# Kernel tuning notes

Measured on AMD Instinct MI355X. Metric: run time of the kernel, lower is better.

Reference implementation:

```python
import jax, jax.numpy as jnp
import numpy as np

N_NODES = 50000
N_EDGES = 400000
H = 64          # node hidden state dim (entities_dimensions['node'])
E_DIM = 8       # edge_params dim (message.extra_parameters)
MSG_HID = 128   # message-creation MLP hidden width
RD_HID = 128    # readout hidden width
T = 2           # message-passing steps


def setup_inputs() -> dict:
    key = jax.random.key(0)
    ks = jax.random.split(key, 12)
    def w(k, shape):
        return jax.random.normal(k, shape, dtype=jnp.float32) * 0.05
    return {
        "node_feats": jax.random.normal(ks[0], (N_NODES, H), dtype=jnp.float32),
        "edge_feats": jax.random.normal(ks[1], (N_EDGES, E_DIM), dtype=jnp.float32),
        "edge_src": jax.random.randint(ks[2], (N_EDGES,), 0, N_NODES),
        "edge_dst": jax.random.randint(ks[3], (N_EDGES,), 0, N_NODES),
        # message creation MLP: concat(hs_src, hs_dst, edge_params) -> relu -> H
        "W_msg1": w(ks[4], (2 * H + E_DIM, MSG_HID)),
        "b_msg1": jnp.zeros((MSG_HID,), jnp.float32),
        "W_msg2": w(ks[5], (MSG_HID, H)),
        "b_msg2": jnp.zeros((H,), jnp.float32),
        # GRU cell update (keras GRUCell convention, reset_after=False)
        "W_x": w(ks[6], (H, 3 * H)),
        "W_h": w(ks[7], (H, 3 * H)),
        "b_gru": jnp.zeros((3 * H,), jnp.float32),
        # readout MLP: H -> relu -> 1
        "W_r1": w(ks[8], (H, RD_HID)),
        "b_r1": jnp.zeros((RD_HID,), jnp.float32),
        "W_r2": w(ks[9], (RD_HID, 1)),
        "b_r2": jnp.zeros((1,), jnp.float32),
    }


def _gru_cell(h, x, W_x, W_h, b):
    # gates order: update (z), reset (r), candidate (h~) — keras convention
    gx = x @ W_x + b
    gh = h @ W_h
    xz, xr, xh = jnp.split(gx, 3, axis=-1)
    hz, hr, hh = jnp.split(gh, 3, axis=-1)
    z = jax.nn.sigmoid(xz + hz)
    r = jax.nn.sigmoid(xr + hr)
    hc = jnp.tanh(xh + r * hh)
    return z * h + (1.0 - z) * hc


def reference(node_feats, edge_feats, edge_src, edge_dst,
              W_msg1, b_msg1, W_msg2, b_msg2,
              W_x, W_h, b_gru, W_r1, b_r1, W_r2, b_r2):
    h = node_feats  # [N, H] hidden states initialized from entity features
    for _ in range(T):
        # gather source/destination node states per edge: [E, H]
        src_h = h[edge_src]
        dst_h = h[edge_dst]
        m_in = jnp.concatenate([src_h, dst_h, edge_feats], axis=-1)  # [E, 2H+E_DIM]
        m = jax.nn.relu(m_in @ W_msg1 + b_msg1) @ W_msg2 + b_msg2    # [E, H]
        # scatter-sum aggregation to destination nodes: [N, H]
        agg = jax.ops.segment_sum(m, edge_dst, num_segments=N_NODES)
        # recurrent (GRU) node-state update
        h = _gru_cell(h, agg, W_x, W_h, b_gru)
    # readout MLP on final hidden states
    out = jax.nn.relu(h @ W_r1 + b_r1) @ W_r2 + b_r2  # [N, 1]
    return out
```

## Files before the change

kernel.cpp:

```cpp
#include <hip/hip_runtime.h>
#include <hip/hip_bf16.h>

#define NN 50000
#define NE 400000
#define NPAIR 12500
#define NCH 196
#define NPAD 50176

typedef __bf16 bf16_t;
typedef __bf16 bf16x4 __attribute__((ext_vector_type(4)));
typedef __bf16 bf16x8 __attribute__((ext_vector_type(8)));
typedef float  floatx4 __attribute__((ext_vector_type(4)));

static __device__ __forceinline__ floatx4 mfma16(bf16x8 a, bf16x8 b, floatx4 c) {
    return __builtin_amdgcn_mfma_f32_16x16x32_bf16(a, b, c, 0, 0, 0);
}
static __device__ __forceinline__ float sigm_f(float x) {
    return 1.f / (1.f + __expf(-x));
}
static __device__ __forceinline__ float tanh_f(float x) {
    return 1.f - 2.f / (__expf(2.f * x) + 1.f);
}
static __device__ __forceinline__ bf16x8 cvt8(const float* sp) {
    float4 f0 = *(const float4*)sp;
    float4 f1 = *(const float4*)(sp + 4);
    bf16x8 v;
    v[0] = (bf16_t)f0.x; v[1] = (bf16_t)f0.y; v[2] = (bf16_t)f0.z; v[3] = (bf16_t)f0.w;
    v[4] = (bf16_t)f1.x; v[5] = (bf16_t)f1.y; v[6] = (bf16_t)f1.z; v[7] = (bf16_t)f1.w;
    return v;
}

__global__ __launch_bounds__(256) void prep_kernel(
    const float* __restrict__ nf,
    const float* __restrict__ Wm1, const float* __restrict__ Wm2,
    const float* __restrict__ Wx,  const float* __restrict__ Wh,
    const float* __restrict__ Wr1,
    bf16_t* __restrict__ hb,
    bf16_t* __restrict__ W1f, bf16_t* __restrict__ W2f,
    bf16_t* __restrict__ Wxt, bf16_t* __restrict__ Wht,
    bf16_t* __restrict__ Wr1f)
{
    int u = blockIdx.x * 256 + threadIdx.x;
    if (u < 800000) {
        float4 v = *(const float4*)(nf + (size_t)u * 4);
        bf16x4 o;
        o[0] = (bf16_t)v.x; o[1] = (bf16_t)v.y; o[2] = (bf16_t)v.z; o[3] = (bf16_t)v.w;
        *(bf16x4*)(hb + (size_t)u * 4) = o;
        return;
    }
    u -= 800000;
    if (u < 20480) {
        int j = u & 7, l = (u >> 3) & 63, rem = u >> 9;
        int ks = rem % 5, nt = rem / 5;
        int n = nt * 16 + (l & 15);
        int k = ks * 32 + (l >> 4) * 8 + j;
        W1f[u] = (k < 136) ? (bf16_t)Wm1[k * 128 + n] : (bf16_t)0.f;
        return;
    }
    u -= 20480;
    if (u < 8192) {
        int j = u & 7, l = (u >> 3) & 63, rem = u >> 9;
        int kg = rem & 3, nt = rem >> 2;
        int n = nt * 16 + (l & 15);
        int k = kg * 32 + (l >> 4) * 8 + j;
        W2f[u] = (bf16_t)Wm2[k * 64 + n];
        return;
    }
    u -= 8192;
    if (u < 12288) {
        int n = u >> 6, k = u & 63;
        Wxt[u] = (bf16_t)Wx[k * 192 + n];
        return;
    }
    u -= 12288;
    if (u < 12288) {
        int n = u >> 6, k = u & 63;
        Wht[u] = (bf16_t)Wh[k * 192 + n];
        return;
    }
    u -= 12288;
    if (u < 8192) {
        int j = u & 7, l = (u >> 3) & 63, rem = u >> 9;
        int kg = rem & 1, nt = rem >> 1;
        int n = nt * 16 + (l & 15);
        int k = kg * 32 + (l >> 4) * 8 + j;
        Wr1f[u] = (bf16_t)Wr1[k * 128 + n];
    }
}

__global__ __launch_bounds__(256) void hist_kernel(
    const int* __restrict__ edst, int* __restrict__ deg)
{
    int e = blockIdx.x * 256 + threadIdx.x;
    if (e < NE) atomicAdd(&deg[edst[e]], 1);
}

__global__ __launch_bounds__(256) void scanA_kernel(
    const int* __restrict__ deg, int* __restrict__ chunkSums)
{
    __shared__ int s[256];
    int i = blockIdx.x * 256 + threadIdx.x;
    s[threadIdx.x] = deg[i];
    __syncthreads();
    for (int st = 128; st >= 1; st >>= 1) {
        if (threadIdx.x < st) s[threadIdx.x] += s[threadIdx.x + st];
        __syncthreads();
    }
    if (threadIdx.x == 0) chunkSums[blockIdx.x] = s[0];
}

__global__ __launch_bounds__(256) void scanB_kernel(
    const int* __restrict__ chunkSums, int* __restrict__ chunkOff)
{
    __shared__ int s[256];
    int t = threadIdx.x;
    int v = (t < NCH) ? chunkSums[t] : 0;
    s[t] = v;
    __syncthreads();
    for (int st = 1; st < 256; st <<= 1) {
        int add = (t >= st) ? s[t - st] : 0;
        __syncthreads();
        s[t] += add;
        __syncthreads();
    }
    if (t < NCH) chunkOff[t] = s[t] - v;
}

__global__ __launch_bounds__(256) void scanC_kernel(
    const int* __restrict__ deg, const int* __restrict__ chunkOff,
    int* __restrict__ cursor)
{
    __shared__ int s[256];
    int t = threadIdx.x;
    int i = blockIdx.x * 256 + t;
    int v = deg[i];
    s[t] = v;
    __syncthreads();
    for (int st = 1; st < 256; st <<= 1) {
        int add = (t >= st) ? s[t - st] : 0;
        __syncthreads();
        s[t] += add;
        __syncthreads();
    }
    cursor[i] = chunkOff[blockIdx.x] + s[t] - v;
}

__global__ __launch_bounds__(256) void scatter_kernel(
    const int* __restrict__ esrc, const int* __restrict__ edst,
    const float* __restrict__ ef,
    int* __restrict__ cursor, int* __restrict__ srcs, int* __restrict__ dsts,
    bf16_t* __restrict__ efpb)
{
    int e = blockIdx.x * 256 + threadIdx.x;
    if (e >= NE) return;
    int d = edst[e];
    int p = atomicAdd(&cursor[d], 1);
    srcs[p] = esrc[e];
    dsts[p] = d;
    float4 a = *(const float4*)(ef + (size_t)e * 8);
    float4 b = *(const float4*)(ef + (size_t)e * 8 + 4);
    bf16x8 v;
    v[0] = (bf16_t)a.x; v[1] = (bf16_t)a.y; v[2] = (bf16_t)a.z; v[3] = (bf16_t)a.w;
    v[4] = (bf16_t)b.x; v[5] = (bf16_t)b.y; v[6] = (bf16_t)b.z; v[7] = (bf16_t)b.w;
    *(bf16x8*)(efpb + (size_t)p * 8) = v;
}

__global__ __launch_bounds__(256) void edge_kernel(
    const bf16_t* __restrict__ hb, const bf16_t* __restrict__ efpb,
    const int* __restrict__ srcs, const int* __restrict__ dsts,
    const bf16_t* __restrict__ W1f, const bf16_t* __restrict__ W2f,
    const float* __restrict__ b1f, const float* __restrict__ b2f,
    bf16_t* __restrict__ mb)
{
    __shared__ __attribute__((aligned(16))) bf16_t w1s[20480];
    __shared__ __attribute__((aligned(16))) bf16_t w2s[8192];
    __shared__ __attribute__((aligned(16))) bf16_t hq[4][32 * 36];

    const int tid = threadIdx.x;
    {
        const uint4* s1 = (const uint4*)W1f;
        uint4* d1 = (uint4*)w1s;
        #pragma unroll
        for (int i = 0; i < 10; i++) d1[tid + i * 256] = s1[tid + i * 256];
        const uint4* s2 = (const uint4*)W2f;
        uint4* d2 = (uint4*)w2s;
        #pragma unroll
        for (int i = 0; i < 4; i++) d2[tid + i * 256] = s2[tid + i * 256];
    }
    __syncthreads();

    const int lane = tid & 63;
    const int wv   = tid >> 6;
    const int l15  = lane & 15;
    const int quad = lane >> 4;

    float b1r[8], b2r[4];
    #pragma unroll
    for (int nt = 0; nt < 8; nt++) b1r[nt] = b1f[nt * 16 + l15];
    #pragma unroll
    for (int nt = 0; nt < 4; nt++) b2r[nt] = b2f[nt * 16 + l15];

    const int WTOT = gridDim.x * 4;

    auto LDIDX = [&](int pp, int* idx) {
        int b = pp * 32;
        idx[0] = srcs[b + l15];       idx[1] = dsts[b + l15];
        idx[2] = srcs[b + 16 + l15];  idx[3] = dsts[b + 16 + l15];
    };
    auto GATHER = [&](const int* idx, int pp, bf16x8* af) {
        const bf16_t* sp0 = hb + (size_t)idx[0] * 64 + quad * 8;
        const bf16_t* dp0 = hb + (size_t)idx[1] * 64 + quad * 8;
        const bf16_t* sp1 = hb + (size_t)idx[2] * 64 + quad * 8;
        const bf16_t* dp1 = hb + (size_t)idx[3] * 64 + quad * 8;
        af[0] = *(const bf16x8*)sp0;  af[1] = *(const bf16x8*)(sp0 + 32);
        af[2] = *(const bf16x8*)dp0;  af[3] = *(const bf16x8*)(dp0 + 32);
        af[5] = *(const bf16x8*)sp1;  af[6] = *(const bf16x8*)(sp1 + 32);
        af[7] = *(const bf16x8*)dp1;  af[8] = *(const bf16x8*)(dp1 + 32);
        if (quad == 0) {
            int b = pp * 32;
            af[4] = *(const bf16x8*)(efpb + (size_t)(b + l15) * 8);
            af[9] = *(const bf16x8*)(efpb + (size_t)(b + 16 + l15) * 8);
        }
    };
    auto COMPSTORE = [&](const bf16x8* af, int pcur) {
        floatx4 oa0[4], oa1[4];
        #pragma unroll
        for (int nt = 0; nt < 4; nt++) {
            oa0[nt].x=0.f; oa0[nt].y=0.f; oa0[nt].z=0.f; oa0[nt].w=0.f;
            oa1[nt].x=0.f; oa1[nt].y=0.f; oa1[nt].z=0.f; oa1[nt].w=0.f;
        }
        #pragma unroll
        for (int q = 0; q < 4; q++) {
            floatx4 ac0[2], ac1[2];
            #pragma unroll
            for (int nt = 0; nt < 2; nt++) {
                ac0[nt].x=0.f; ac0[nt].y=0.f; ac0[nt].z=0.f; ac0[nt].w=0.f;
                ac1[nt].x=0.f; ac1[nt].y=0.f; ac1[nt].z=0.f; ac1[nt].w=0.f;
            }
            #pragma unroll
            for (int nt = 0; nt < 2; nt++) {
                int gnt = q * 2 + nt;
                #pragma unroll
                for (int ks = 0; ks < 5; ks++) {
                    bf16x8 b = *(const bf16x8*)(w1s + ((gnt * 5 + ks) * 64 + lane) * 8);
                    ac0[nt] = mfma16(af[ks], b, ac0[nt]);
                    ac1[nt] = mfma16(af[5 + ks], b, ac1[nt]);
                }
            }
            #pragma unroll
            for (int nt = 0; nt < 2; nt++) {
                float bb = b1r[q * 2 + nt];
                #pragma unroll
                for (int r = 0; r < 4; r++) {
                    float v0 = fmaxf(ac0[nt][r] + bb, 0.f);
                    float v1 = fmaxf(ac1[nt][r] + bb, 0.f);
                    hq[wv][(quad * 4 + r) * 36 + nt * 16 + l15]      = (bf16_t)v0;
                    hq[wv][(16 + quad * 4 + r) * 36 + nt * 16 + l15] = (bf16_t)v1;
                }
            }
            bf16x8 hf0 = *(const bf16x8*)(hq[wv] + l15 * 36 + quad * 8);
            bf16x8 hf1 = *(const bf16x8*)(hq[wv] + (16 + l15) * 36 + quad * 8);
            #pragma unroll
            for (int nt = 0; nt < 4; nt++) {
                bf16x8 w2 = *(const bf16x8*)(w2s + ((nt * 4 + q) * 64 + lane) * 8);
                oa0[nt] = mfma16(hf0, w2, oa0[nt]);
                oa1[nt] = mfma16(hf1, w2, oa1[nt]);
            }
        }
        int base = pcur * 32;
        #pragma unroll
        for (int nt = 0; nt < 4; nt++) {
            int col = nt * 16 + l15;
            float bb = b2r[nt];
            #pragma unroll
            for (int r = 0; r < 4; r++) {
                int row0 = base + quad * 4 + r;
                int row1 = base + 16 + quad * 4 + r;
                mb[(size_t)row0 * 64 + col] = (bf16_t)(oa0[nt][r] + bb);
                mb[(size_t)row1 * 64 + col] = (bf16_t)(oa1[nt][r] + bb);
            }
        }
    };

    int p = blockIdx.x * 4 + wv;
    int iA[4], iB[4];
    bf16x8 afA[10], afB[10];
    if (quad != 0) {
        #pragma unroll
        for (int q = 0; q < 8; q++) {
            afA[4][q] = (bf16_t)0.f; afA[9][q] = (bf16_t)0.f;
            afB[4][q] = (bf16_t)0.f; afB[9][q] = (bf16_t)0.f;
        }
    }

    LDIDX(p, iA);
    GATHER(iA, p, afA);
    int pn = p + WTOT;
    int pp = (pn < NPAIR) ? pn : p;
    LDIDX(pp, iB);

    while (true) {
        GATHER(iB, pp, afB);
        {
            int pn2 = pn + WTOT;
            int pq  = (pn2 < NPAIR) ? pn2 : pp;
            LDIDX(pq, iA);
            COMPSTORE(afA, p);
            if (pn >= NPAIR) break;
            p = pn; pn = pn2; pp = pq;
        }
        GATHER(iA, pp, afA);
        {
            int pn2 = pn + WTOT;
            int pq  = (pn2 < NPAIR) ? pn2 : pp;
            LDIDX(pq, iB);
            COMPSTORE(afB, p);
            if (pn >= NPAIR) break;
            p = pn; pn = pn2; pp = pq;
        }
    }
}

__global__ __launch_bounds__(256) void agg_kernel(
    const bf16_t* __restrict__ mb, const int* __restrict__ deg,
    const int* __restrict__ cursor, bf16_t* __restrict__ aggb)
{
    const int node = blockIdx.x * 4 + (threadIdx.x >> 6);
    if (node >= NN) return;
    const int lane = threadIdx.x & 63;
    int dg  = deg[node];
    int end = cursor[node];
    int st  = end - dg;
    float s0 = 0.f, s1 = 0.f;
    int e = st;
    for (; e + 1 < end; e += 2) {
        s0 += (float)mb[(size_t)e * 64 + lane];
        s1 += (float)mb[(size_t)(e + 1) * 64 + lane];
    }
    if (e < end) s0 += (float)mb[(size_t)e * 64 + lane];
    aggb[(size_t)node * 64 + lane] = (bf16_t)(s0 + s1);
}

template<int LAST>
__global__ __launch_bounds__(256) void gru_kernel(
    const bf16_t* __restrict__ aggb, const float* __restrict__ h_in,
    float* __restrict__ h_out, bf16_t* __restrict__ hb_out,
    const bf16_t* __restrict__ Wxt, const bf16_t* __restrict__ Wht,
    const float* __restrict__ bg,
    const bf16_t* __restrict__ Wr1f, const float* __restrict__ br1,
    const float* __restrict__ Wr2, const float* __restrict__ br2,
    float* __restrict__ out)
{
    __shared__ __attribute__((aligned(16))) float  shd[64 * 68];
    __shared__ __attribute__((aligned(16))) bf16_t hb2[4][16 * 72];
    const int tid = threadIdx.x;
    const int n0  = blockIdx.x * 64;

    for (int idx = tid; idx < 64 * 16; idx += 256) {
        int i = idx >> 4, c = (idx & 15) * 4;
        int n = n0 + i; if (n >= NN) n = NN - 1;
        *(float4*)&shd[i * 68 + c] = *(const float4*)(h_in + (size_t)n * 64 + c);
    }
    __syncthreads();

    const int lane = tid & 63;
    const int wv   = tid >> 6;
    const int l15  = lane & 15;
    const int quad = lane >> 4;
    const int rowA = wv * 16 + l15;
    int nA = n0 + rowA; if (nA >= NN) nA = NN - 1;

    bf16x8 ax[2], ah[2];
    ax[0] = *(const bf16x8*)(aggb + (size_t)nA * 64 + quad * 8);
    ax[1] = *(const bf16x8*)(aggb + (size_t)nA * 64 + quad * 8 + 32);
    {
        const float* hp = shd + rowA * 68 + quad * 8;
        ah[0] = cvt8(hp);
        ah[1] = cvt8(hp + 32);
    }

    floatx4 az[4], ar[4], axh[4], ahh[4];
    #pragma unroll
    for (int nt = 0; nt < 4; nt++) {
        az[nt].x=0.f; az[nt].y=0.f; az[nt].z=0.f; az[nt].w=0.f;
        ar[nt].x=0.f; ar[nt].y=0.f; ar[nt].z=0.f; ar[nt].w=0.f;
        axh[nt].x=0.f; axh[nt].y=0.f; axh[nt].z=0.f; axh[nt].w=0.f;
        ahh[nt].x=0.f; ahh[nt].y=0.f; ahh[nt].z=0.f; ahh[nt].w=0.f;
    }
    #pragma unroll
    for (int nt = 0; nt < 4; nt++) {
        const bf16_t* bx_z = Wxt + (nt * 16 + l15) * 64 + quad * 8;
        const bf16_t* bh_z = Wht + (nt * 16 + l15) * 64 + quad * 8;
        const bf16_t* bx_r = bx_z + 64 * 64;
        const bf16_t* bh_r = bh_z + 64 * 64;
        const bf16_t* bx_h = bx_z + 128 * 64;
        const bf16_t* bh_h = bh_z + 128 * 64;
        az[nt]  = mfma16(ax[0], *(const bf16x8*)bx_z,        az[nt]);
        az[nt]  = mfma16(ax[1], *(const bf16x8*)(bx_z + 32), az[nt]);
        az[nt]  = mfma16(ah[0], *(const bf16x8*)bh_z,        az[nt]);
        az[nt]  = mfma16(ah[1], *(const bf16x8*)(bh_z + 32), az[nt]);
        ar[nt]  = mfma16(ax[0], *(const bf16x8*)bx_r,        ar[nt]);
        ar[nt]  = mfma16(ax[1], *(const bf16x8*)(bx_r + 32), ar[nt]);
        ar[nt]  = mfma16(ah[0], *(const bf16x8*)bh_r,        ar[nt]);
        ar[nt]  = mfma16(ah[1], *(const bf16x8*)(bh_r + 32), ar[nt]);
        axh[nt] = mfma16(ax[0], *(const bf16x8*)bx_h,        axh[nt]);
        axh[nt] = mfma16(ax[1], *(const bf16x8*)(bx_h + 32), axh[nt]);
        ahh[nt] = mfma16(ah[0], *(const bf16x8*)bh_h,        ahh[nt]);
        ahh[nt] = mfma16(ah[1], *(const bf16x8*)(bh_h + 32), ahh[nt]);
    }

    #pragma unroll
    for (int nt = 0; nt < 4; nt++) {
        int j = nt * 16 + l15;
        float bz = bg[j], brr = bg[64 + j], bh = bg[128 + j];
        #pragma unroll
        for (int r = 0; r < 4; r++) {
            int lrow = wv * 16 + quad * 4 + r;
            int n = n0 + lrow;
            float z  = sigm_f(az[nt][r] + bz);
            float rr = sigm_f(ar[nt][r] + brr);
            float hc = tanh_f(axh[nt][r] + bh + rr * ahh[nt][r]);
            float hold = shd[lrow * 68 + j];
            float hnew = z * hold + (1.f - z) * hc;
            if (LAST) {
                hb2[wv][(quad * 4 + r) * 72 + j] = (bf16_t)hnew;
            } else if (n < NN) {
                h_out[(size_t)n * 64 + j]  = hnew;
                hb_out[(size_t)n * 64 + j] = (bf16_t)hnew;
            }
        }
    }

    if (LAST) {
        bf16x8 a0 = *(const bf16x8*)(hb2[wv] + l15 * 72 + quad * 8);
        bf16x8 a1 = *(const bf16x8*)(hb2[wv] + l15 * 72 + quad * 8 + 32);
        floatx4 accR[8];
        #pragma unroll
        for (int nt = 0; nt < 8; nt++) { accR[nt].x=0.f; accR[nt].y=0.f; accR[nt].z=0.f; accR[nt].w=0.f; }
        #pragma unroll
        for (int nt = 0; nt < 8; nt++) {
            bf16x8 b0 = *(const bf16x8*)(Wr1f + ((nt * 2 + 0) * 64 + lane) * 8);
            bf16x8 b1 = *(const bf16x8*)(Wr1f + ((nt * 2 + 1) * 64 + lane) * 8);
            accR[nt] = mfma16(a0, b0, accR[nt]);
            accR[nt] = mfma16(a1, b1, accR[nt]);
        }
        float br1r[8], wr2r[8];
        #pragma unroll
        for (int nt = 0; nt < 8; nt++) {
            br1r[nt] = br1[nt * 16 + l15];
            wr2r[nt] = Wr2[nt * 16 + l15];
        }
        float br2v = br2[0];
        #pragma unroll
        for (int r = 0; r < 4; r++) {
            float p = 0.f;
            #pragma unroll
            for (int nt = 0; nt < 8; nt++)
                p += fmaxf(accR[nt][r] + br1r[nt], 0.f) * wr2r[nt];
            p += __shfl_xor(p, 1, 64);
            p += __shfl_xor(p, 2, 64);
            p += __shfl_xor(p, 4, 64);
            p += __shfl_xor(p, 8, 64);
            if (l15 == 0) {
                int n = n0 + wv * 16 + quad * 4 + r;
                if (n < NN) out[n] = p + br2v;
            }
        }
    }
}

extern "C" void kernel_launch(void* const* d_in, const int* in_sizes, int n_in,
                              void* d_out, int out_size, void* d_ws, size_t ws_size,
                              hipStream_t stream)
{
    const float* nf  = (const float*)d_in[0];
    const float* ef  = (const float*)d_in[1];
    const int* esrc  = (const int*)d_in[2];
    const int* edst  = (const int*)d_in[3];
    const float* Wm1 = (const float*)d_in[4];
    const float* bm1 = (const float*)d_in[5];
    const float* Wm2 = (const float*)d_in[6];
    const float* bm2 = (const float*)d_in[7];
    const float* Wx  = (const float*)d_in[8];
    const float* Wh  = (const float*)d_in[9];
    const float* bg  = (const float*)d_in[10];
    const float* Wr1 = (const float*)d_in[11];
    const float* br1 = (const float*)d_in[12];
    const float* Wr2 = (const float*)d_in[13];
    const float* br2 = (const float*)d_in[14];

    char* ws = (char*)d_ws;
    float*  hbuf   = (float*)(ws);
    bf16_t* hb     = (bf16_t*)(ws + 12800000);
    bf16_t* W1f    = (bf16_t*)(ws + 19200000);
    bf16_t* W2f    = (bf16_t*)(ws + 19240960);
    bf16_t* Wxt    = (bf16_t*)(ws + 19257344);
    bf16_t* Wht    = (bf16_t*)(ws + 19281920);
    bf16_t* Wr1f   = (bf16_t*)(ws + 19306496);
    int*    srcs   = (int*)(ws + 19322880);
    int*    dsts   = (int*)(ws + 20922880);
    bf16_t* efpb   = (bf16_t*)(ws + 22522880);
    int*    deg    = (int*)(ws + 28922880);
    int*    cursor = (int*)(ws + 29123584);
    int*    chunkS = (int*)(ws + 29324288);
    int*    chunkO = (int*)(ws + 29325312);
    bf16_t* aggb   = (bf16_t*)(ws + 29326336);
    bf16_t* mb     = (bf16_t*)(ws + 35726336);

    prep_kernel<<<3365, 256, 0, stream>>>(nf, Wm1, Wm2, Wx, Wh, Wr1,
                                          hb, W1f, W2f, Wxt, Wht, Wr1f);

    hipMemsetAsync(deg, 0, (size_t)NPAD * 4, stream);
    hist_kernel<<<(NE + 255) / 256, 256, 0, stream>>>(edst, deg);
    scanA_kernel<<<NCH, 256, 0, stream>>>(deg, chunkS);
    scanB_kernel<<<1, 256, 0, stream>>>(chunkS, chunkO);
    scanC_kernel<<<NCH, 256, 0, stream>>>(deg, chunkO, cursor);
    scatter_kernel<<<(NE + 255) / 256, 256, 0, stream>>>(esrc, edst, ef, cursor,
                                                         srcs, dsts, efpb);

    edge_kernel<<<1024, 256, 0, stream>>>(hb, efpb, srcs, dsts,
                                          W1f, W2f, bm1, bm2, mb);
    agg_kernel<<<(NN + 3) / 4, 256, 0, stream>>>(mb, deg, cursor, aggb);
    gru_kernel<0><<<(NN + 63) / 64, 256, 0, stream>>>(
        aggb, nf, hbuf, hb, Wxt, Wht, bg, Wr1f, br1, Wr2, br2, (float*)d_out);
    edge_kernel<<<1024, 256, 0, stream>>>(hb, efpb, srcs, dsts,
                                          W1f, W2f, bm1, bm2, mb);
    agg_kernel<<<(NN + 3) / 4, 256, 0, stream>>>(mb, deg, cursor, aggb);
    gru_kernel<1><<<(NN + 63) / 64, 256, 0, stream>>>(
        aggb, hbuf, nullptr, nullptr, Wxt, Wht, bg, Wr1f, br1, Wr2, br2,
        (float*)d_out);
}
```

Baseline: 318.5 us.

## Store messages in permuted column layout for vectorized writes and aggregation reads

The message-creation epilogue now stores each lane's four column-tile outputs as one contiguous bf16x4 write, which permutes the column order in the intermediate message buffer. The aggregation kernel reads that layout with 8-byte vector loads, gives each wave quarter a different edge, and combines the four partial sums with cross-lane shuffles before un-permuting on store. The goal is fewer, wider stores and loads on the message buffer plus more edges in flight per node. In exchange it adds a shuffle reduction, and three quarters of the lanes sit idle during the final store.

```diff
diff --git a/kernel.cpp b/kernel.cpp
--- a/kernel.cpp
+++ b/kernel.cpp
@@ -269,16 +269,20 @@
         }
         int base = pcur * 32;
         #pragma unroll
-        for (int nt = 0; nt < 4; nt++) {
-            int col = nt * 16 + l15;
-            float bb = b2r[nt];
-            #pragma unroll
-            for (int r = 0; r < 4; r++) {
-                int row0 = base + quad * 4 + r;
-                int row1 = base + 16 + quad * 4 + r;
-                mb[(size_t)row0 * 64 + col] = (bf16_t)(oa0[nt][r] + bb);
-                mb[(size_t)row1 * 64 + col] = (bf16_t)(oa1[nt][r] + bb);
-            }
+        for (int r = 0; r < 4; r++) {
+            int row0 = base + quad * 4 + r;
+            int row1 = base + 16 + quad * 4 + r;
+            bf16x4 t0, t1;
+            t0[0] = (bf16_t)(oa0[0][r] + b2r[0]);
+            t0[1] = (bf16_t)(oa0[1][r] + b2r[1]);
+            t0[2] = (bf16_t)(oa0[2][r] + b2r[2]);
+            t0[3] = (bf16_t)(oa0[3][r] + b2r[3]);
+            t1[0] = (bf16_t)(oa1[0][r] + b2r[0]);
+            t1[1] = (bf16_t)(oa1[1][r] + b2r[1]);
+            t1[2] = (bf16_t)(oa1[2][r] + b2r[2]);
+            t1[3] = (bf16_t)(oa1[3][r] + b2r[3]);
+            *(bf16x4*)(mb + (size_t)row0 * 64 + l15 * 4) = t0;
+            *(bf16x4*)(mb + (size_t)row1 * 64 + l15 * 4) = t1;
         }
     };
 
@@ -328,17 +332,26 @@
     const int node = blockIdx.x * 4 + (threadIdx.x >> 6);
     if (node >= NN) return;
     const int lane = threadIdx.x & 63;
+    const int l15  = lane & 15;
+    const int quad = lane >> 4;
     int dg  = deg[node];
     int end = cursor[node];
     int st  = end - dg;
-    float s0 = 0.f, s1 = 0.f;
-    int e = st;
-    for (; e + 1 < end; e += 2) {
-        s0 += (float)mb[(size_t)e * 64 + lane];
-        s1 += (float)mb[(size_t)(e + 1) * 64 + lane];
-    }
-    if (e < end) s0 += (float)mb[(size_t)e * 64 + lane];
-    aggb[(size_t)node * 64 + lane] = (bf16_t)(s0 + s1);
+    float a0 = 0.f, a1 = 0.f, a2 = 0.f, a3 = 0.f;
+    for (int e = st + quad; e < end; e += 4) {
+        bf16x4 v = *(const bf16x4*)(mb + (size_t)e * 64 + l15 * 4);
+        a0 += (float)v[0]; a1 += (float)v[1]; a2 += (float)v[2]; a3 += (float)v[3];
+    }
+    a0 += __shfl_xor(a0, 16, 64); a0 += __shfl_xor(a0, 32, 64);
+    a1 += __shfl_xor(a1, 16, 64); a1 += __shfl_xor(a1, 32, 64);
+    a2 += __shfl_xor(a2, 16, 64); a2 += __shfl_xor(a2, 32, 64);
+    a3 += __shfl_xor(a3, 16, 64); a3 += __shfl_xor(a3, 32, 64);
+    if (quad == 0) {
+        aggb[(size_t)node * 64 +      l15] = (bf16_t)a0;
+        aggb[(size_t)node * 64 + 16 + l15] = (bf16_t)a1;
+        aggb[(size_t)node * 64 + 32 + l15] = (bf16_t)a2;
+        aggb[(size_t)node * 64 + 48 + l15] = (bf16_t)a3;
+    }
 }
 
 template<int LAST>
```

Result: no change. 315.7 us (-0.9%).
